# Kernel tuning notes

Measured on AMD Instinct MI355X. Metric: run time of the kernel, lower is better.

Reference implementation:

```python
import jax, jax.numpy as jnp
import numpy as np

B, S, H = 2, 2048, 1024
E, K, F = 64, 8, 512
NORM_TOPK = True
CAP_FACTOR = 2.0


def setup_inputs() -> dict:
    key = jax.random.key(0)
    k0, k1, k2, k3, k4 = jax.random.split(key, 5)
    s_h = 1.0 / np.sqrt(H)
    s_f = 1.0 / np.sqrt(F)
    return {
        "hidden_states": jax.random.normal(k0, (B, S, H), jnp.float32),
        "w_gate": jax.random.normal(k1, (H, E), jnp.float32) * s_h,  # gate: Linear(H->E), no bias
        "w1": jax.random.normal(k2, (E, H, F), jnp.float32) * s_h,   # gate_proj per expert
        "w3": jax.random.normal(k3, (E, H, F), jnp.float32) * s_h,   # up_proj per expert
        "w2": jax.random.normal(k4, (E, F, H), jnp.float32) * s_f,   # down_proj per expert
    }


def reference(hidden_states, w_gate, w1, w3, w2):
    b, s, h = hidden_states.shape
    e = w_gate.shape[1]
    t = b * s
    x = hidden_states.reshape(t, h)
    router_logits = x @ w_gate                                   # [T, E]
    probs = jax.nn.softmax(router_logits.astype(jnp.float32), axis=-1)
    topw, sel = jax.lax.top_k(probs, K)                          # [T, K]
    if NORM_TOPK:
        topw = topw / jnp.sum(topw, axis=-1, keepdims=True)
    topw = topw.astype(x.dtype)

    a = t * K                                                    # total assignments
    c = int(CAP_FACTOR * a / e)                                  # static per-expert capacity
    sel_flat = sel.reshape(a)
    w_flat = topw.reshape(a)
    tok = jnp.repeat(jnp.arange(t), K)
    order = jnp.argsort(sel_flat, stable=True)                   # group assignments by expert
    e_s, t_s, w_s = sel_flat[order], tok[order], w_flat[order]
    counts = jnp.bincount(sel_flat, length=e)
    starts = jnp.cumsum(counts) - counts
    pos = jnp.arange(a) - starts[e_s]                            # position within expert group
    valid = pos < c
    slot = jnp.where(valid, e_s * c + pos, e * c)                # overflow -> dropped sentinel slot

    # dispatch: gather tokens into per-expert contiguous buffer [E, C, H]
    buf = jnp.zeros((e * c + 1, h), x.dtype).at[slot].set(x[t_s])
    xb = buf[: e * c].reshape(e, c, h)
    # grouped gated-SiLU MLP per expert
    g = jnp.einsum('ech,ehf->ecf', xb, w1)
    u = jnp.einsum('ech,ehf->ecf', xb, w3)
    yb = jnp.einsum('ecf,efh->ech', jax.nn.silu(g) * u, w2).reshape(e * c, h)
    # combine: weighted scatter-add back to tokens
    contrib = yb[jnp.minimum(slot, e * c - 1)] * (w_s * valid.astype(x.dtype))[:, None]
    out = jnp.zeros((t, h), x.dtype).at[t_s].add(contrib)
    return out.reshape(b, s, h), router_logits
```

## Files before the change

kernel.cpp:

```cpp
#include <hip/hip_runtime.h>
#include <hip/hip_bf16.h>

#define T_TOK 4096
#define H_DIM 1024
#define E_EXP 64
#define TOPK  8
#define F_DIM 512
#define CAP   1024
#define A_TOT (T_TOK * TOPK)

typedef _Float16 f16;
typedef _Float16 f16x8 __attribute__((ext_vector_type(8)));
typedef float    f32x4 __attribute__((ext_vector_type(4)));

__global__ __launch_bounds__(256) void pack_w_kernel(
    const float* __restrict__ src, f16* __restrict__ dst, int Kd, int Nd)
{
    const int tid  = threadIdx.x;
    const int lane = tid & 63, wv = tid >> 6;
    const int kbs = __builtin_ctz(Kd >> 5);
    const int nts = __builtin_ctz(Nd >> 4);
    const int chunk = blockIdx.x * 4 + wv;
    const int kt = chunk & ((1 << kbs) - 1);
    const int en = chunk >> kbs;
    const int nt = en & ((1 << nts) - 1);
    const int e  = en >> nts;
    const int jj = lane & 15, qq = lane >> 4;
    const float* s = src + ((size_t)e * Kd + kt * 32 + qq * 8) * Nd + nt * 16 + jj;
    f16x8 v;
    #pragma unroll
    for (int j = 0; j < 8; ++j) v[j] = (f16)s[(size_t)j * Nd];
    *(f16x8*)(dst + (size_t)chunk * 512 + lane * 8) = v;
}

__global__ __launch_bounds__(256) void router_kernel(
    const float* __restrict__ x, const float* __restrict__ wg,
    float* __restrict__ logits_out, int* __restrict__ sel,
    float* __restrict__ wgtA, f16* __restrict__ xh)
{
    __shared__ float xs[16][128];
    __shared__ float ls[16][65];
    const int tid = threadIdx.x;
    const int e  = tid & 63;
    const int tg = tid >> 6;
    const int tb = blockIdx.x * 16;

    float acc[4] = {0.f, 0.f, 0.f, 0.f};
    for (int h0 = 0; h0 < H_DIM; h0 += 128) {
        {
            int r  = tid >> 4;
            int c0 = (tid & 15) * 8;
            const float4* src = (const float4*)(x + (size_t)(tb + r) * H_DIM + h0 + c0);
            float4 v0 = src[0], v1 = src[1];
            *(float4*)&xs[r][c0]     = v0;
            *(float4*)&xs[r][c0 + 4] = v1;
            f16x8 hv;
            hv[0] = (f16)v0.x; hv[1] = (f16)v0.y; hv[2] = (f16)v0.z; hv[3] = (f16)v0.w;
            hv[4] = (f16)v1.x; hv[5] = (f16)v1.y; hv[6] = (f16)v1.z; hv[7] = (f16)v1.w;
            *(f16x8*)(xh + (size_t)(tb + r) * H_DIM + h0 + c0) = hv;
        }
        __syncthreads();
        for (int hh = 0; hh < 128; ++hh) {
            float w = wg[(size_t)(h0 + hh) * E_EXP + e];
            #pragma unroll
            for (int i = 0; i < 4; ++i)
                acc[i] = fmaf(xs[tg * 4 + i][hh], w, acc[i]);
        }
        __syncthreads();
    }
    #pragma unroll
    for (int i = 0; i < 4; ++i) {
        int tt = tg * 4 + i;
        logits_out[(size_t)(tb + tt) * E_EXP + e] = acc[i];
        ls[tt][e] = acc[i];
    }
    __syncthreads();
    if (tid < 16) {
        int tt = tid;
        float lv[8]; int li[8];
        for (int k = 0; k < 8; ++k) {
            float m = -1e30f; int mi = 0;
            for (int j = 0; j < 64; ++j) {
                float v = ls[tt][j];
                if (v > m) { m = v; mi = j; }
            }
            lv[k] = m; li[k] = mi;
            ls[tt][mi] = -1e30f;
        }
        float s = 0.f, wv[8];
        for (int k = 0; k < 8; ++k) { wv[k] = __expf(lv[k] - lv[0]); s += wv[k]; }
        float inv = 1.f / s;
        for (int k = 0; k < 8; ++k) {
            int a = (tb + tt) * TOPK + k;
            sel[a]  = li[k];
            wgtA[a] = wv[k] * inv;
        }
    }
}

__global__ __launch_bounds__(256) void build_lists_kernel(
    const int* __restrict__ sel,
    int* __restrict__ tok_list, int* __restrict__ slotA,
    int* __restrict__ counts)
{
    __shared__ int sc[256];
    const int e = blockIdx.x;
    const int tid = threadIdx.x;
    const int per = A_TOT / 256;
    const int a0 = tid * per;
    int cnt = 0;
    for (int i = 0; i < per; ++i) cnt += (sel[a0 + i] == e) ? 1 : 0;
    sc[tid] = cnt;
    __syncthreads();
    for (int s = 1; s < 256; s <<= 1) {
        int v = (tid >= s) ? sc[tid - s] : 0;
        __syncthreads();
        sc[tid] += v;
        __syncthreads();
    }
    int total = sc[255];
    int pos = sc[tid] - cnt;
    if (tid == 0) counts[e] = (total < CAP) ? total : CAP;
    for (int i = 0; i < per; ++i) {
        int a = a0 + i;
        if (sel[a] == e) {
            if (pos < CAP) {
                tok_list[e * CAP + pos] = a >> 3;
                slotA[a] = e * CAP + pos;
            } else {
                slotA[a] = -1;
            }
            pos++;
        }
    }
}

#define MFMA16(a, b, c) __builtin_amdgcn_mfma_f32_16x16x32_f16(a, b, c, 0, 0, 0)

__global__ __launch_bounds__(256) void gemm1_kernel(
    const f16* __restrict__ xh, const f16* __restrict__ w1p,
    const f16* __restrict__ w3p, const int* __restrict__ tok_list,
    const int* __restrict__ counts, f16* __restrict__ P)
{
    const int id = blockIdx.x;
    const int x7 = id & 7, r = id >> 3;
    const int ft = r & 3, mt = (r >> 2) & 15, eh = r >> 6;
    const int e = x7 + 8 * eh;
    const int cnt = counts[e];
    const int m0 = mt * 64;
    if (m0 >= cnt) return;
    const int bf = ft * 128;

    __shared__ f16 Xs[2][64][64];
    __shared__ int tok_s[64];

    const int tid = threadIdx.x;
    const int lane = tid & 63, wv = tid >> 6;
    const int jj = lane & 15, qq = lane >> 4;
    const int sr = tid >> 3, sc = (tid & 7) * 8;
    const int swz_w = ((tid & 7) ^ (sr & 7)) * 8;
    const int x8 = jj & 7;
    const int s0 = (qq ^ x8) * 8;
    const int s1 = ((qq + 4) ^ x8) * 8;

    if (tid < 64) {
        int m = m0 + tid;
        tok_s[tid] = (m < cnt) ? tok_list[e * CAP + m] : tok_list[e * CAP];
    }
    __syncthreads();
    const size_t rowA = (size_t)tok_s[sr] * H_DIM + sc;
    const size_t rowB = (size_t)tok_s[sr + 32] * H_DIM + sc;

    const int ntA = ft * 8 + wv * 2;
    const f16* w1a = w1p + ((size_t)(e * 32 + ntA) * 32) * 512 + lane * 8;
    const f16* w3a = w3p + ((size_t)(e * 32 + ntA) * 32) * 512 + lane * 8;

    f32x4 accG[4][2], accU[4][2];
    #pragma unroll
    for (int i = 0; i < 4; ++i)
        #pragma unroll
        for (int n = 0; n < 2; ++n) {
            accG[i][n] = (f32x4){0.f, 0.f, 0.f, 0.f};
            accU[i][n] = (f32x4){0.f, 0.f, 0.f, 0.f};
        }

    {
        f16x8 a = *(const f16x8*)(xh + rowA);
        f16x8 b = *(const f16x8*)(xh + rowB);
        *(f16x8*)&Xs[0][sr][swz_w]      = a;
        *(f16x8*)&Xs[0][sr + 32][swz_w] = b;
    }
    f16x8 cG[4], cU[4];
    cG[0] = *(const f16x8*)(w1a);
    cG[1] = *(const f16x8*)(w1a + 512);
    cG[2] = *(const f16x8*)(w1a + 16384);
    cG[3] = *(const f16x8*)(w1a + 16384 + 512);
    cU[0] = *(const f16x8*)(w3a);
    cU[1] = *(const f16x8*)(w3a + 512);
    cU[2] = *(const f16x8*)(w3a + 16384);
    cU[3] = *(const f16x8*)(w3a + 16384 + 512);

    #pragma unroll
    for (int it = 0; it < 16; ++it) {
        const int k0 = it * 64;
        __syncthreads();
        f16x8 xn0, xn1, nG[4], nU[4];
        if (it < 15) {
            xn0 = *(const f16x8*)(xh + rowA + k0 + 64);
            xn1 = *(const f16x8*)(xh + rowB + k0 + 64);
            size_t kg = (size_t)(2 * it + 2) * 512;
            nG[0] = *(const f16x8*)(w1a + kg);
            nG[1] = *(const f16x8*)(w1a + kg + 512);
            nG[2] = *(const f16x8*)(w1a + kg + 16384);
            nG[3] = *(const f16x8*)(w1a + kg + 16384 + 512);
            nU[0] = *(const f16x8*)(w3a + kg);
            nU[1] = *(const f16x8*)(w3a + kg + 512);
            nU[2] = *(const f16x8*)(w3a + kg + 16384);
            nU[3] = *(const f16x8*)(w3a + kg + 16384 + 512);
        }
        const int buf = it & 1;
        #pragma unroll
        for (int m2 = 0; m2 < 4; ++m2) {
            f16x8 a0 = *(const f16x8*)&Xs[buf][m2 * 16 + jj][s0];
            f16x8 a1 = *(const f16x8*)&Xs[buf][m2 * 16 + jj][s1];
            accG[m2][0] = MFMA16(a0, cG[0], accG[m2][0]);
            accG[m2][0] = MFMA16(a1, cG[1], accG[m2][0]);
            accG[m2][1] = MFMA16(a0, cG[2], accG[m2][1]);
            accG[m2][1] = MFMA16(a1, cG[3], accG[m2][1]);
            accU[m2][0] = MFMA16(a0, cU[0], accU[m2][0]);
            accU[m2][0] = MFMA16(a1, cU[1], accU[m2][0]);
            accU[m2][1] = MFMA16(a0, cU[2], accU[m2][1]);
            accU[m2][1] = MFMA16(a1, cU[3], accU[m2][1]);
        }
        if (it < 15) {
            *(f16x8*)&Xs[buf ^ 1][sr][swz_w]      = xn0;
            *(f16x8*)&Xs[buf ^ 1][sr + 32][swz_w] = xn1;
            #pragma unroll
            for (int i = 0; i < 4; ++i) { cG[i] = nG[i]; cU[i] = nU[i]; }
        }
    }
    #pragma unroll
    for (int m2 = 0; m2 < 4; ++m2) {
        #pragma unroll
        for (int n = 0; n < 2; ++n) {
            #pragma unroll
            for (int rr = 0; rr < 4; ++rr) {
                int row = m2 * 16 + qq * 4 + rr;
                float gg = accG[m2][n][rr], u = accU[m2][n][rr];
                float p = gg / (1.f + __expf(-gg)) * u;
                P[(size_t)(e * CAP + m0 + row) * F_DIM + bf + (wv * 2 + n) * 16 + jj] = (f16)p;
            }
        }
    }
}

__global__ __launch_bounds__(256) void gemm2_kernel(
    const f16* __restrict__ P, const f16* __restrict__ w2p,
    const int* __restrict__ counts, f16* __restrict__ Y)
{
    const int id = blockIdx.x;
    const int x7 = id & 7, r = id >> 3;
    const int ht = r & 3, mt = (r >> 2) & 15, eh = r >> 6;
    const int e = x7 + 8 * eh;
    const int cnt = counts[e];
    const int m0 = mt * 64;
    if (m0 >= cnt) return;
    const int h0 = ht * 256;

    __shared__ f16 Ps[2][64][64];

    const int tid = threadIdx.x;
    const int lane = tid & 63, wv = tid >> 6;
    const int jj = lane & 15, qq = lane >> 4;
    const int sr = tid >> 3, sc = (tid & 7) * 8;
    const int swz_w = ((tid & 7) ^ (sr & 7)) * 8;
    const int x8 = jj & 7;
    const int s0 = (qq ^ x8) * 8;
    const int s1 = ((qq + 4) ^ x8) * 8;

    const size_t pbase = (size_t)(e * CAP + m0) * F_DIM;
    const int nt0 = ht * 16 + wv * 4;
    const f16* wb = w2p + ((size_t)(e * 64 + nt0) * 16) * 512 + lane * 8;

    f32x4 acc[4][4];
    #pragma unroll
    for (int i = 0; i < 4; ++i)
        #pragma unroll
        for (int n = 0; n < 4; ++n)
            acc[i][n] = (f32x4){0.f, 0.f, 0.f, 0.f};

    {
        f16x8 a = *(const f16x8*)(P + pbase + (size_t)sr * F_DIM + sc);
        f16x8 b = *(const f16x8*)(P + pbase + (size_t)(sr + 32) * F_DIM + sc);
        *(f16x8*)&Ps[0][sr][swz_w]      = a;
        *(f16x8*)&Ps[0][sr + 32][swz_w] = b;
    }
    f16x8 cW[8];
    #pragma unroll
    for (int i = 0; i < 4; ++i) {
        cW[i * 2]     = *(const f16x8*)(wb + (size_t)i * 8192);
        cW[i * 2 + 1] = *(const f16x8*)(wb + (size_t)i * 8192 + 512);
    }

    #pragma unroll
    for (int it = 0; it < 8; ++it) {
        const int k0 = it * 64;
        __syncthreads();
        f16x8 pn0, pn1, nW[8];
        if (it < 7) {
            pn0 = *(const f16x8*)(P + pbase + (size_t)sr * F_DIM + k0 + 64 + sc);
            pn1 = *(const f16x8*)(P + pbase + (size_t)(sr + 32) * F_DIM + k0 + 64 + sc);
            size_t kg = (size_t)(2 * it + 2) * 512;
            #pragma unroll
            for (int i = 0; i < 4; ++i) {
                nW[i * 2]     = *(const f16x8*)(wb + (size_t)i * 8192 + kg);
                nW[i * 2 + 1] = *(const f16x8*)(wb + (size_t)i * 8192 + kg + 512);
            }
        }
        const int buf = it & 1;
        #pragma unroll
        for (int m2 = 0; m2 < 4; ++m2) {
            f16x8 a0 = *(const f16x8*)&Ps[buf][m2 * 16 + jj][s0];
            f16x8 a1 = *(const f16x8*)&Ps[buf][m2 * 16 + jj][s1];
            #pragma unroll
            for (int i = 0; i < 4; ++i) {
                acc[m2][i] = MFMA16(a0, cW[i * 2],     acc[m2][i]);
                acc[m2][i] = MFMA16(a1, cW[i * 2 + 1], acc[m2][i]);
            }
        }
        if (it < 7) {
            *(f16x8*)&Ps[buf ^ 1][sr][swz_w]      = pn0;
            *(f16x8*)&Ps[buf ^ 1][sr + 32][swz_w] = pn1;
            #pragma unroll
            for (int i = 0; i < 8; ++i) cW[i] = nW[i];
        }
    }
    f16* yb = Y + (size_t)(e * CAP + m0) * H_DIM + h0 + wv * 64 + jj;
    #pragma unroll
    for (int m2 = 0; m2 < 4; ++m2) {
        #pragma unroll
        for (int rr = 0; rr < 4; ++rr) {
            int row = m2 * 16 + qq * 4 + rr;
            #pragma unroll
            for (int i = 0; i < 4; ++i)
                yb[(size_t)row * H_DIM + i * 16] = (f16)acc[m2][i][rr];
        }
    }
}

__global__ __launch_bounds__(256) void combine_kernel(
    const f16* __restrict__ Y, const int* __restrict__ slotA,
    const float* __restrict__ wgtA, float* __restrict__ out)
{
    const int tid = threadIdx.x;
    const int t  = blockIdx.x * 2 + (tid >> 7);
    const int hc = (tid & 127) * 8;
    float acc[8] = {0.f, 0.f, 0.f, 0.f, 0.f, 0.f, 0.f, 0.f};
    const int base = t * TOPK;
    #pragma unroll
    for (int k = 0; k < 8; ++k) {
        int s   = slotA[base + k];
        float w = wgtA[base + k];
        if (s >= 0) {
            f16x8 y = *(const f16x8*)(Y + (size_t)s * H_DIM + hc);
            #pragma unroll
            for (int j = 0; j < 8; ++j) acc[j] += w * (float)y[j];
        }
    }
    float4 o0 = {acc[0], acc[1], acc[2], acc[3]};
    float4 o1 = {acc[4], acc[5], acc[6], acc[7]};
    *(float4*)(out + (size_t)t * H_DIM + hc)     = o0;
    *(float4*)(out + (size_t)t * H_DIM + hc + 4) = o1;
}

extern "C" void kernel_launch(void* const* d_in, const int* in_sizes, int n_in,
                              void* d_out, int out_size, void* d_ws, size_t ws_size,
                              hipStream_t stream) {
    const float* x  = (const float*)d_in[0];
    const float* wg = (const float*)d_in[1];
    const float* w1 = (const float*)d_in[2];
    const float* w3 = (const float*)d_in[3];
    const float* w2 = (const float*)d_in[4];

    float* out    = (float*)d_out;
    float* logits = out + (size_t)T_TOK * H_DIM;

    char* ws = (char*)d_ws;
    int*   sel      = (int*)  (ws);
    float* wgtA     = (float*)(ws + (128 << 10));
    int*   tok_list = (int*)  (ws + (256 << 10));
    int*   slotA    = (int*)  (ws + (512 << 10));
    int*   counts   = (int*)  (ws + (768 << 10));
    f16*   xh       = (f16*)  (ws + (size_t)(1 << 20));
    f16*   P        = (f16*)  (ws + (size_t)(9 << 20));
    f16*   w1p      = (f16*)  (ws + (size_t)(73 << 20));
    f16*   w3p      = (f16*)  (ws + (size_t)(137 << 20));
    f16*   w2p      = (f16*)  (ws + (size_t)(201 << 20));
    f16*   Y        = (f16*)  (ws + (size_t)(73 << 20));

    pack_w_kernel<<<16384, 256, 0, stream>>>(w1, w1p, H_DIM, F_DIM);
    pack_w_kernel<<<16384, 256, 0, stream>>>(w3, w3p, H_DIM, F_DIM);
    pack_w_kernel<<<16384, 256, 0, stream>>>(w2, w2p, F_DIM, H_DIM);
    router_kernel<<<T_TOK / 16, 256, 0, stream>>>(x, wg, logits, sel, wgtA, xh);
    build_lists_kernel<<<E_EXP, 256, 0, stream>>>(sel, tok_list, slotA, counts);
    gemm1_kernel<<<4096, 256, 0, stream>>>(xh, w1p, w3p, tok_list, counts, P);
    gemm2_kernel<<<4096, 256, 0, stream>>>(P, w2p, counts, Y);
    combine_kernel<<<T_TOK / 2, 256, 0, stream>>>(Y, slotA, wgtA, out);
}
```

Measured before the change: 684.1 us.

## Use 128-row tiles with 8 waves per block in expert GEMMs; merge weight packing launches

The grouped GEMM kernels now use 512-thread blocks with a 4x2 wave grid covering 128 token rows instead of 64. The N-width per block is halved so the grid size stays the same. This doubles reuse of each expert weight tile across tokens and halves redundant weight traffic. The three weight-pack launches are merged into one kernel that picks its source tensor by chunk index, saving launch overhead. In exchange the 128-row tiles waste more work on partially filled expert groups, and larger blocks may reduce occupancy.

```diff
diff --git a/kernel.cpp b/kernel.cpp
--- a/kernel.cpp
+++ b/kernel.cpp
@@ -13,16 +13,22 @@
 typedef _Float16 f16x8 __attribute__((ext_vector_type(8)));
 typedef float    f32x4 __attribute__((ext_vector_type(4)));
 
-__global__ __launch_bounds__(256) void pack_w_kernel(
-    const float* __restrict__ src, f16* __restrict__ dst, int Kd, int Nd)
+__global__ __launch_bounds__(256) void pack_all_kernel(
+    const float* __restrict__ w1, const float* __restrict__ w3,
+    const float* __restrict__ w2,
+    f16* __restrict__ w1p, f16* __restrict__ w3p, f16* __restrict__ w2p)
 {
     const int tid  = threadIdx.x;
     const int lane = tid & 63, wv = tid >> 6;
+    int cid = blockIdx.x * 4 + wv;
+    const float* src; f16* dst; int Kd, Nd;
+    if (cid < 65536)       { src = w1; dst = w1p; Kd = 1024; Nd = 512; }
+    else if (cid < 131072) { src = w3; dst = w3p; Kd = 1024; Nd = 512; cid -= 65536; }
+    else                   { src = w2; dst = w2p; Kd = 512;  Nd = 1024; cid -= 131072; }
     const int kbs = __builtin_ctz(Kd >> 5);
     const int nts = __builtin_ctz(Nd >> 4);
-    const int chunk = blockIdx.x * 4 + wv;
-    const int kt = chunk & ((1 << kbs) - 1);
-    const int en = chunk >> kbs;
+    const int kt = cid & ((1 << kbs) - 1);
+    const int en = cid >> kbs;
     const int nt = en & ((1 << nts) - 1);
     const int e  = en >> nts;
     const int jj = lane & 15, qq = lane >> 4;
@@ -30,7 +36,7 @@
     f16x8 v;
     #pragma unroll
     for (int j = 0; j < 8; ++j) v[j] = (f16)s[(size_t)j * Nd];
-    *(f16x8*)(dst + (size_t)chunk * 512 + lane * 8) = v;
+    *(f16x8*)(dst + (size_t)cid * 512 + (size_t)(blockIdx.x * 4 + wv >= 131072 ? 0 : 0) + lane * 8) = v;
 }
 
 __global__ __launch_bounds__(256) void router_kernel(
@@ -137,47 +143,48 @@
 
 #define MFMA16(a, b, c) __builtin_amdgcn_mfma_f32_16x16x32_f16(a, b, c, 0, 0, 0)
 
-__global__ __launch_bounds__(256) void gemm1_kernel(
+__global__ __launch_bounds__(512) void gemm1_kernel(
     const f16* __restrict__ xh, const f16* __restrict__ w1p,
     const f16* __restrict__ w3p, const int* __restrict__ tok_list,
     const int* __restrict__ counts, f16* __restrict__ P)
 {
     const int id = blockIdx.x;
     const int x7 = id & 7, r = id >> 3;
-    const int ft = r & 3, mt = (r >> 2) & 15, eh = r >> 6;
+    const int ft = r & 7, mt = (r >> 3) & 7, eh = r >> 6;
     const int e = x7 + 8 * eh;
     const int cnt = counts[e];
-    const int m0 = mt * 64;
+    const int m0 = mt * 128;
     if (m0 >= cnt) return;
-    const int bf = ft * 128;
-
-    __shared__ f16 Xs[2][64][64];
-    __shared__ int tok_s[64];
+    const int bf = ft * 64;
+
+    __shared__ f16 Xs[2][128][64];
+    __shared__ int tok_s[128];
 
     const int tid = threadIdx.x;
     const int lane = tid & 63, wv = tid >> 6;
+    const int wm = wv >> 1, wn = wv & 1;
     const int jj = lane & 15, qq = lane >> 4;
     const int sr = tid >> 3, sc = (tid & 7) * 8;
     const int swz_w = ((tid & 7) ^ (sr & 7)) * 8;
-    const int x8 = jj & 7;
+    const int x8 = jj & 15 & 7;
     const int s0 = (qq ^ x8) * 8;
     const int s1 = ((qq + 4) ^ x8) * 8;
 
-    if (tid < 64) {
+    if (tid < 128) {
         int m = m0 + tid;
         tok_s[tid] = (m < cnt) ? tok_list[e * CAP + m] : tok_list[e * CAP];
     }
     __syncthreads();
     const size_t rowA = (size_t)tok_s[sr] * H_DIM + sc;
-    const size_t rowB = (size_t)tok_s[sr + 32] * H_DIM + sc;
-
-    const int ntA = ft * 8 + wv * 2;
+    const size_t rowB = (size_t)tok_s[sr + 64] * H_DIM + sc;
+
+    const int ntA = ft * 4 + wn * 2;
     const f16* w1a = w1p + ((size_t)(e * 32 + ntA) * 32) * 512 + lane * 8;
     const f16* w3a = w3p + ((size_t)(e * 32 + ntA) * 32) * 512 + lane * 8;
 
-    f32x4 accG[4][2], accU[4][2];
-    #pragma unroll
-    for (int i = 0; i < 4; ++i)
+    f32x4 accG[2][2], accU[2][2];
+    #pragma unroll
+    for (int i = 0; i < 2; ++i)
         #pragma unroll
         for (int n = 0; n < 2; ++n) {
             accG[i][n] = (f32x4){0.f, 0.f, 0.f, 0.f};
@@ -188,7 +195,7 @@
         f16x8 a = *(const f16x8*)(xh + rowA);
         f16x8 b = *(const f16x8*)(xh + rowB);
         *(f16x8*)&Xs[0][sr][swz_w]      = a;
-        *(f16x8*)&Xs[0][sr + 32][swz_w] = b;
+        *(f16x8*)&Xs[0][sr + 64][swz_w] = b;
     }
     f16x8 cG[4], cU[4];
     cG[0] = *(const f16x8*)(w1a);
@@ -220,9 +227,9 @@
         }
         const int buf = it & 1;
         #pragma unroll
-        for (int m2 = 0; m2 < 4; ++m2) {
-            f16x8 a0 = *(const f16x8*)&Xs[buf][m2 * 16 + jj][s0];
-            f16x8 a1 = *(const f16x8*)&Xs[buf][m2 * 16 + jj][s1];
+        for (int m2 = 0; m2 < 2; ++m2) {
+            f16x8 a0 = *(const f16x8*)&Xs[buf][wm * 32 + m2 * 16 + jj][s0];
+            f16x8 a1 = *(const f16x8*)&Xs[buf][wm * 32 + m2 * 16 + jj][s1];
             accG[m2][0] = MFMA16(a0, cG[0], accG[m2][0]);
             accG[m2][0] = MFMA16(a1, cG[1], accG[m2][0]);
             accG[m2][1] = MFMA16(a0, cG[2], accG[m2][1]);
@@ -234,43 +241,44 @@
         }
         if (it < 15) {
             *(f16x8*)&Xs[buf ^ 1][sr][swz_w]      = xn0;
-            *(f16x8*)&Xs[buf ^ 1][sr + 32][swz_w] = xn1;
+            *(f16x8*)&Xs[buf ^ 1][sr + 64][swz_w] = xn1;
             #pragma unroll
             for (int i = 0; i < 4; ++i) { cG[i] = nG[i]; cU[i] = nU[i]; }
         }
     }
     #pragma unroll
-    for (int m2 = 0; m2 < 4; ++m2) {
+    for (int m2 = 0; m2 < 2; ++m2) {
         #pragma unroll
         for (int n = 0; n < 2; ++n) {
             #pragma unroll
             for (int rr = 0; rr < 4; ++rr) {
-                int row = m2 * 16 + qq * 4 + rr;
+                int row = wm * 32 + m2 * 16 + qq * 4 + rr;
                 float gg = accG[m2][n][rr], u = accU[m2][n][rr];
                 float p = gg / (1.f + __expf(-gg)) * u;
-                P[(size_t)(e * CAP + m0 + row) * F_DIM + bf + (wv * 2 + n) * 16 + jj] = (f16)p;
+                P[(size_t)(e * CAP + m0 + row) * F_DIM + bf + (wn * 2 + n) * 16 + jj] = (f16)p;
             }
         }
     }
 }
 
-__global__ __launch_bounds__(256) void gemm2_kernel(
+__global__ __launch_bounds__(512) void gemm2_kernel(
     const f16* __restrict__ P, const f16* __restrict__ w2p,
     const int* __restrict__ counts, f16* __restrict__ Y)
 {
     const int id = blockIdx.x;
     const int x7 = id & 7, r = id >> 3;
-    const int ht = r & 3, mt = (r >> 2) & 15, eh = r >> 6;
+    const int ht = r & 7, mt = (r >> 3) & 7, eh = r >> 6;
     const int e = x7 + 8 * eh;
     const int cnt = counts[e];
-    const int m0 = mt * 64;
+    const int m0 = mt * 128;
     if (m0 >= cnt) return;
-    const int h0 = ht * 256;
-
-    __shared__ f16 Ps[2][64][64];
+    const int h0 = ht * 128;
+
+    __shared__ f16 Ps[2][128][64];
 
     const int tid = threadIdx.x;
     const int lane = tid & 63, wv = tid >> 6;
+    const int wm = wv >> 1, wn = wv & 1;
     const int jj = lane & 15, qq = lane >> 4;
     const int sr = tid >> 3, sc = (tid & 7) * 8;
     const int swz_w = ((tid & 7) ^ (sr & 7)) * 8;
@@ -279,21 +287,21 @@
     const int s1 = ((qq + 4) ^ x8) * 8;
 
     const size_t pbase = (size_t)(e * CAP + m0) * F_DIM;
-    const int nt0 = ht * 16 + wv * 4;
+    const int nt0 = ht * 8 + wn * 4;
     const f16* wb = w2p + ((size_t)(e * 64 + nt0) * 16) * 512 + lane * 8;
 
-    f32x4 acc[4][4];
-    #pragma unroll
-    for (int i = 0; i < 4; ++i)
+    f32x4 acc[2][4];
+    #pragma unroll
+    for (int i = 0; i < 2; ++i)
         #pragma unroll
         for (int n = 0; n < 4; ++n)
             acc[i][n] = (f32x4){0.f, 0.f, 0.f, 0.f};
 
     {
         f16x8 a = *(const f16x8*)(P + pbase + (size_t)sr * F_DIM + sc);
-        f16x8 b = *(const f16x8*)(P + pbase + (size_t)(sr + 32) * F_DIM + sc);
+        f16x8 b = *(const f16x8*)(P + pbase + (size_t)(sr + 64) * F_DIM + sc);
         *(f16x8*)&Ps[0][sr][swz_w]      = a;
-        *(f16x8*)&Ps[0][sr + 32][swz_w] = b;
+        *(f16x8*)&Ps[0][sr + 64][swz_w] = b;
     }
     f16x8 cW[8];
     #pragma unroll
@@ -309,7 +317,7 @@
         f16x8 pn0, pn1, nW[8];
         if (it < 7) {
             pn0 = *(const f16x8*)(P + pbase + (size_t)sr * F_DIM + k0 + 64 + sc);
-            pn1 = *(const f16x8*)(P + pbase + (size_t)(sr + 32) * F_DIM + k0 + 64 + sc);
+            pn1 = *(const f16x8*)(P + pbase + (size_t)(sr + 64) * F_DIM + k0 + 64 + sc);
             size_t kg = (size_t)(2 * it + 2) * 512;
             #pragma unroll
             for (int i = 0; i < 4; ++i) {
@@ -319,9 +327,9 @@
         }
         const int buf = it & 1;
         #pragma unroll
-        for (int m2 = 0; m2 < 4; ++m2) {
-            f16x8 a0 = *(const f16x8*)&Ps[buf][m2 * 16 + jj][s0];
-            f16x8 a1 = *(const f16x8*)&Ps[buf][m2 * 16 + jj][s1];
+        for (int m2 = 0; m2 < 2; ++m2) {
+            f16x8 a0 = *(const f16x8*)&Ps[buf][wm * 32 + m2 * 16 + jj][s0];
+            f16x8 a1 = *(const f16x8*)&Ps[buf][wm * 32 + m2 * 16 + jj][s1];
             #pragma unroll
             for (int i = 0; i < 4; ++i) {
                 acc[m2][i] = MFMA16(a0, cW[i * 2],     acc[m2][i]);
@@ -330,17 +338,17 @@
         }
         if (it < 7) {
             *(f16x8*)&Ps[buf ^ 1][sr][swz_w]      = pn0;
-            *(f16x8*)&Ps[buf ^ 1][sr + 32][swz_w] = pn1;
+            *(f16x8*)&Ps[buf ^ 1][sr + 64][swz_w] = pn1;
             #pragma unroll
             for (int i = 0; i < 8; ++i) cW[i] = nW[i];
         }
     }
-    f16* yb = Y + (size_t)(e * CAP + m0) * H_DIM + h0 + wv * 64 + jj;
-    #pragma unroll
-    for (int m2 = 0; m2 < 4; ++m2) {
+    f16* yb = Y + (size_t)(e * CAP + m0) * H_DIM + h0 + wn * 64 + jj;
+    #pragma unroll
+    for (int m2 = 0; m2 < 2; ++m2) {
         #pragma unroll
         for (int rr = 0; rr < 4; ++rr) {
-            int row = m2 * 16 + qq * 4 + rr;
+            int row = wm * 32 + m2 * 16 + qq * 4 + rr;
             #pragma unroll
             for (int i = 0; i < 4; ++i)
                 yb[(size_t)row * H_DIM + i * 16] = (f16)acc[m2][i][rr];
@@ -398,12 +406,10 @@
     f16*   w2p      = (f16*)  (ws + (size_t)(201 << 20));
     f16*   Y        = (f16*)  (ws + (size_t)(73 << 20));
 
-    pack_w_kernel<<<16384, 256, 0, stream>>>(w1, w1p, H_DIM, F_DIM);
-    pack_w_kernel<<<16384, 256, 0, stream>>>(w3, w3p, H_DIM, F_DIM);
-    pack_w_kernel<<<16384, 256, 0, stream>>>(w2, w2p, F_DIM, H_DIM);
+    pack_all_kernel<<<49152, 256, 0, stream>>>(w1, w3, w2, w1p, w3p, w2p);
     router_kernel<<<T_TOK / 16, 256, 0, stream>>>(x, wg, logits, sel, wgtA, xh);
     build_lists_kernel<<<E_EXP, 256, 0, stream>>>(sel, tok_list, slotA, counts);
-    gemm1_kernel<<<4096, 256, 0, stream>>>(xh, w1p, w3p, tok_list, counts, P);
-    gemm2_kernel<<<4096, 256, 0, stream>>>(P, w2p, counts, Y);
+    gemm1_kernel<<<4096, 512, 0, stream>>>(xh, w1p, w3p, tok_list, counts, P);
+    gemm2_kernel<<<4096, 512, 0, stream>>>(P, w2p, counts, Y);
     combine_kernel<<<T_TOK / 2, 256, 0, stream>>>(Y, slotA, wgtA, out);
 }
```

Result: slower. 701.9 us (+2.6%).
